# Optimization experiments

Hardware: AMD Instinct MI355X
Metric: run time of the kernel (lower is better)

## Reference

```python
import jax, jax.numpy as jnp
import numpy as np

B, T = 64, 2048
D_RNN, D_EMB, D_ATT = 1024, 512, 128
N_FILT, KSIZE = 32, 31
PAD = (KSIZE - 1) // 2


def setup_inputs() -> dict:
    key = jax.random.key(0)
    ks = jax.random.split(key, 9)
    return {
        "attention_hidden_state": jax.random.normal(ks[0], (B, D_RNN), jnp.float32),
        "memory": jax.random.normal(ks[1], (B, T, D_EMB), jnp.float32),
        "processed_memory": jax.random.normal(ks[2], (B, T, D_ATT), jnp.float32),
        "attention_weights_cat": jax.random.uniform(ks[3], (B, 2, T), jnp.float32),
        "mask": jax.random.randint(ks[4], (B, T), 0, 2) > 0,
        # learned params (all bias-free, as in the torch module)
        "Wq": jax.random.normal(ks[5], (D_ATT, D_RNN), jnp.float32) * 0.02,   # query_layer.weight
        "Wv": jax.random.normal(ks[6], (1, D_ATT), jnp.float32) * 0.02,        # v.weight
        "conv_w": jax.random.normal(ks[7], (N_FILT, 2, KSIZE), jnp.float32) * 0.1,  # location_conv.weight (OIH)
        "Wd": jax.random.normal(ks[8], (D_ATT, N_FILT), jnp.float32) * 0.02,   # location_dense.weight
    }


def reference(attention_hidden_state, memory, processed_memory,
              attention_weights_cat, mask, Wq, Wv, conv_w, Wd):
    # processed query: [B, 1, D_ATT]
    pq = (attention_hidden_state @ Wq.T)[:, None, :]
    # location features: Conv1d(2 -> N_FILT, same padding) over time
    loc = jax.lax.conv_general_dilated(
        attention_weights_cat, conv_w,
        window_strides=(1,), padding=[(PAD, PAD)],
        dimension_numbers=("NCH", "OIH", "NCH"))           # [B, N_FILT, T]
    paw = jnp.einsum("bft,af->bta", loc, Wd)               # [B, T, D_ATT]
    # additive energies -> scalar per position via v-projection
    energies = jnp.einsum("bta,a->bt", jnp.tanh(pq + paw + processed_memory), Wv[0])
    alignment = jnp.where(mask, -jnp.inf, energies)         # masked fill
    attention_weights = jax.nn.softmax(alignment, axis=1)   # [B, T]
    attention_context = jnp.einsum("bt,btd->bd", attention_weights, memory)  # [B, D_EMB]
    return attention_context, jax.lax.stop_gradient(attention_weights)
```

## Files before the change

### kernel.cpp

```cpp
#include <hip/hip_runtime.h>
#include <math.h>

#define B_    64
#define T_    2048
#define DRNN  1024
#define DEMB  512
#define DATT  128
#define NF    32
#define KS    31
#define PADL  15
#define MP    64
#define TT    32
#define CT    64
#define NC    (T_/CT)

__device__ __forceinline__ float fast_tanh(float x){
    float e2 = __expf(2.0f * x);
    return 1.0f - 2.0f / (e2 + 1.0f);
}

__global__ __launch_bounds__(128) void prep_kernel(
    const float* __restrict__ hidden, const float* __restrict__ Wq,
    const float* __restrict__ Wd, const float* __restrict__ convw,
    float* __restrict__ pq, float* __restrict__ M)
{
    const int blk = blockIdx.x;
    const int a = threadIdx.x;
    if (blk < B_) {
        __shared__ float sh[DRNN];
        const int b = blk;
        #pragma unroll
        for (int i = 0; i < DRNN/128; ++i) sh[a + 128*i] = hidden[b*DRNN + a + 128*i];
        __syncthreads();
        const float4* wq4 = (const float4*)(Wq + a*DRNN);
        float acc = 0.f;
        #pragma unroll 4
        for (int k = 0; k < DRNN/4; ++k){
            float4 w = wq4[k];
            acc = fmaf(w.x, sh[4*k+0], acc);
            acc = fmaf(w.y, sh[4*k+1], acc);
            acc = fmaf(w.z, sh[4*k+2], acc);
            acc = fmaf(w.w, sh[4*k+3], acc);
        }
        pq[b*DATT + a] = acc;
    } else {
        float wd[NF];
        #pragma unroll
        for (int f = 0; f < NF; ++f) wd[f] = Wd[a*NF + f];
        for (int ck = 0; ck < 2*KS; ++ck){
            float acc = 0.f;
            #pragma unroll
            for (int f = 0; f < NF; ++f) acc = fmaf(wd[f], convw[f*2*KS + ck], acc);
            M[a*MP + ck] = acc;
        }
    }
}

__global__ __launch_bounds__(256) void fused_kernel(
    const float* __restrict__ pm, const float* __restrict__ awcat,
    const float* __restrict__ pq, const float* __restrict__ M,
    const float* __restrict__ Wv, const int* __restrict__ mask,
    const float* __restrict__ memory,
    float* __restrict__ pbuf, float* __restrict__ pmax,
    float* __restrict__ psum, float* __restrict__ pctx)
{
    const int b   = blockIdx.y;
    const int cx  = blockIdx.x;
    const int t0  = cx * CT;
    const int tid = threadIdx.x;
    const int s   = tid >> 7;
    const int a   = tid & 127;
    const int ts  = t0 + TT * s;

    __shared__ float saw0[96], saw1[96];
    __shared__ float sred[2][2][TT];
    __shared__ float2 swt[CT];
    __shared__ int   scount;
    __shared__ float4 sacc[128];

    for (int i = tid; i < 94; i += 256){
        int tt = t0 - PADL + i;
        bool ok = (tt >= 0) && (tt < T_);
        saw0[i] = ok ? awcat[(b*2+0)*T_ + tt] : 0.f;
        saw1[i] = ok ? awcat[(b*2+1)*T_ + tt] : 0.f;
    }
    __syncthreads();

    const float pqa = pq[b*DATT + a];
    const float wv  = Wv[a];
    const float* pmb = pm + ((size_t)(b*T_ + ts)) * DATT + a;

    float acc[TT];
    #pragma unroll
    for (int t = 0; t < TT; ++t) acc[t] = pqa + pmb[(size_t)t * DATT];

    float Ma0[KS], Ma1[KS];
    const float* Mrow = M + a*MP;
    #pragma unroll
    for (int k = 0; k < KS; ++k){ Ma0[k] = Mrow[k]; Ma1[k] = Mrow[KS + k]; }

    #pragma unroll
    for (int j = 0; j < TT + KS - 1; ++j){
        const float av0 = saw0[j + TT*s];
        const float av1 = saw1[j + TT*s];
        const int tlo = (j - KS + 1) > 0 ? (j - KS + 1) : 0;
        const int thi = (j < TT - 1) ? j : (TT - 1);
        #pragma unroll
        for (int t = tlo; t <= thi; ++t){
            acc[t] = fmaf(Ma0[j - t], av0, acc[t]);
            acc[t] = fmaf(Ma1[j - t], av1, acc[t]);
        }
    }

    #pragma unroll
    for (int t = 0; t < TT; ++t){
        acc[t] = wv * fast_tanh(acc[t]);
    }

    const int lane = tid & 63;
    const int half = a >> 6;
    #pragma unroll
    for (int k = 0; k < 16; ++k){
        const bool hi = (lane & 1) != 0;
        float send = hi ? acc[k] : acc[k+16];
        float recv = __shfl_xor(send, 1, 64);
        acc[k] = (hi ? acc[k+16] : acc[k]) + recv;
    }
    #pragma unroll
    for (int k = 0; k < 8; ++k){
        const bool hi = (lane & 2) != 0;
        float send = hi ? acc[k] : acc[k+8];
        float recv = __shfl_xor(send, 2, 64);
        acc[k] = (hi ? acc[k+8] : acc[k]) + recv;
    }
    #pragma unroll
    for (int k = 0; k < 4; ++k){
        const bool hi = (lane & 4) != 0;
        float send = hi ? acc[k] : acc[k+4];
        float recv = __shfl_xor(send, 4, 64);
        acc[k] = (hi ? acc[k+4] : acc[k]) + recv;
    }
    #pragma unroll
    for (int k = 0; k < 2; ++k){
        const bool hi = (lane & 8) != 0;
        float send = hi ? acc[k] : acc[k+2];
        float recv = __shfl_xor(send, 8, 64);
        acc[k] = (hi ? acc[k+2] : acc[k]) + recv;
    }
    {
        const bool hi = (lane & 16) != 0;
        float send = hi ? acc[0] : acc[1];
        float recv = __shfl_xor(send, 16, 64);
        acc[0] = (hi ? acc[1] : acc[0]) + recv;
    }
    acc[0] += __shfl_xor(acc[0], 32, 64);
    const int trev = ((lane & 1) << 4) | (((lane >> 1) & 1) << 3) |
                     (((lane >> 2) & 1) << 2) | (((lane >> 3) & 1) << 1) |
                     ((lane >> 4) & 1);
    if (lane < 32) sred[s][half][trev] = acc[0];
    __syncthreads();

    if (tid < 64){
        const int t = t0 + tid;
        float e = sred[tid>>5][0][tid&31] + sred[tid>>5][1][tid&31];
        const int mk = mask[b*T_ + t];
        float mval = mk ? -1e30f : e;
        #pragma unroll
        for (int off = 1; off < 64; off <<= 1) mval = fmaxf(mval, __shfl_xor(mval, off, 64));
        const float pval = mk ? 0.f : __expf(e - mval);
        float sv = pval;
        #pragma unroll
        for (int off = 1; off < 64; off <<= 1) sv += __shfl_xor(sv, off, 64);
        pbuf[b*T_ + t] = pval;
        const unsigned long long bal = __ballot(pval != 0.f);
        if (pval != 0.f){
            const int pfx = (int)__popcll(bal & ((1ull << tid) - 1ull));
            swt[pfx] = make_float2(pval, __int_as_float(tid));
        }
        if (tid == 0){
            scount = (int)__popcll(bal);
            pmax[b*NC + cx] = mval;
            psum[b*NC + cx] = sv;
        }
    }
    __syncthreads();

    const int n   = scount;
    const int col = tid & 127;
    const int row = tid >> 7;
    float4 a4 = make_float4(0.f, 0.f, 0.f, 0.f);
    const float4* mem4 = (const float4*)memory + ((size_t)(b*T_ + t0))*(DEMB/4) + col;

    int i = row;
    for (; i + 6 < n; i += 8){
        const float2 e0 = swt[i];
        const float2 e1 = swt[i+2];
        const float2 e2 = swt[i+4];
        const float2 e3 = swt[i+6];
        const float4 m0 = mem4[(size_t)__float_as_int(e0.y) * (DEMB/4)];
        const float4 m1 = mem4[(size_t)__float_as_int(e1.y) * (DEMB/4)];
        const float4 m2 = mem4[(size_t)__float_as_int(e2.y) * (DEMB/4)];
        const float4 m3 = mem4[(size_t)__float_as_int(e3.y) * (DEMB/4)];
        a4.x = fmaf(e0.x, m0.x, a4.x); a4.y = fmaf(e0.x, m0.y, a4.y);
        a4.z = fmaf(e0.x, m0.z, a4.z); a4.w = fmaf(e0.x, m0.w, a4.w);
        a4.x = fmaf(e1.x, m1.x, a4.x); a4.y = fmaf(e1.x, m1.y, a4.y);
        a4.z = fmaf(e1.x, m1.z, a4.z); a4.w = fmaf(e1.x, m1.w, a4.w);
        a4.x = fmaf(e2.x, m2.x, a4.x); a4.y = fmaf(e2.x, m2.y, a4.y);
        a4.z = fmaf(e2.x, m2.z, a4.z); a4.w = fmaf(e2.x, m2.w, a4.w);
        a4.x = fmaf(e3.x, m3.x, a4.x); a4.y = fmaf(e3.x, m3.y, a4.y);
        a4.z = fmaf(e3.x, m3.z, a4.z); a4.w = fmaf(e3.x, m3.w, a4.w);
    }
    for (; i < n; i += 2){
        const float2 e = swt[i];
        const float4 m = mem4[(size_t)__float_as_int(e.y) * (DEMB/4)];
        a4.x = fmaf(e.x, m.x, a4.x); a4.y = fmaf(e.x, m.y, a4.y);
        a4.z = fmaf(e.x, m.z, a4.z); a4.w = fmaf(e.x, m.w, a4.w);
    }

    if (row == 1) sacc[col] = a4;
    __syncthreads();
    if (row == 0){
        const float4 o = sacc[col];
        float4* dst = (float4*)(pctx + ((size_t)(b*NC + cx))*DEMB) + col;
        *dst = make_float4(a4.x + o.x, a4.y + o.y, a4.z + o.z, a4.w + o.w);
    }
}

__global__ __launch_bounds__(256) void finalize_kernel(
    const float* __restrict__ pbuf, const float* __restrict__ pmax,
    const float* __restrict__ psum, const float* __restrict__ pctx,
    float* __restrict__ ctx, float* __restrict__ wout)
{
    const int b = blockIdx.x;
    const int tid = threadIdx.x;
    __shared__ float sscale[NC];

    if (tid < 64){
        float mv = (tid < NC) ? pmax[b*NC + tid] : -1e30f;
        float sv = (tid < NC) ? psum[b*NC + tid] : 0.f;
        float g = mv;
        #pragma unroll
        for (int off = 1; off < 64; off <<= 1) g = fmaxf(g, __shfl_xor(g, off, 64));
        float z = sv * __expf(mv - g);
        #pragma unroll
        for (int off = 1; off < 64; off <<= 1) z += __shfl_xor(z, off, 64);
        if (tid < NC) sscale[tid] = __expf(mv - g) / z;
    }
    __syncthreads();

    float2 a2 = make_float2(0.f, 0.f);
    const float2* pc2 = (const float2*)(pctx + (size_t)b*NC*DEMB) + tid;
    #pragma unroll
    for (int c = 0; c < NC; ++c){
        const float sc = sscale[c];
        if (sc != 0.f){
            const float2 v = pc2[(size_t)c * (DEMB/2)];
            a2.x = fmaf(sc, v.x, a2.x);
            a2.y = fmaf(sc, v.y, a2.y);
        }
    }
    ((float2*)(ctx + b*DEMB))[tid] = a2;

    #pragma unroll
    for (int i = 0; i < T_/256; ++i){
        const int t = tid + 256*i;
        wout[b*T_ + t] = pbuf[b*T_ + t] * sscale[t >> 6];
    }
}

extern "C" void kernel_launch(void* const* d_in, const int* in_sizes, int n_in,
                              void* d_out, int out_size, void* d_ws, size_t ws_size,
                              hipStream_t stream)
{
    const float* hidden = (const float*)d_in[0];
    const float* memory = (const float*)d_in[1];
    const float* pm     = (const float*)d_in[2];
    const float* awcat  = (const float*)d_in[3];
    const int*   mask   = (const int*)d_in[4];
    const float* Wq     = (const float*)d_in[5];
    const float* Wv     = (const float*)d_in[6];
    const float* convw  = (const float*)d_in[7];
    const float* Wd     = (const float*)d_in[8];

    float* out  = (float*)d_out;
    float* ctx  = out;
    float* wout = out + B_*DEMB;

    float* pq    = (float*)d_ws;
    float* M     = pq   + B_*DATT;
    float* pbuf  = M    + DATT*MP;
    float* pmax  = pbuf + B_*T_;
    float* psum  = pmax + B_*NC;
    float* pctx  = psum + B_*NC;

    prep_kernel<<<dim3(B_ + 1), 128, 0, stream>>>(hidden, Wq, Wd, convw, pq, M);
    fused_kernel<<<dim3(NC, B_), 256, 0, stream>>>(pm, awcat, pq, M, Wv, mask,
                                                   memory, pbuf, pmax, psum, pctx);
    finalize_kernel<<<dim3(B_), 256, 0, stream>>>(pbuf, pmax, psum, pctx, ctx, wout);
}
```

Baseline: 441.2 us.

## Skip masked processed_memory loads, transpose conv-dense matrix, warp-parallel query projection

The query projection in the prep kernel now uses one wave per group of 32 outputs, with each lane holding a slice of the hidden state in registers and a shuffle reduction, so Wq rows are read coalesced. The combined conv/dense matrix is stored transposed so each thread's per-attention-dim loads are coalesced across threads. In the fused kernel the mask is read once into a ballot bitmask in shared memory, and the processed_memory loads are skipped for masked positions, which cuts roughly half of that traffic. The memory gather loop is also unrolled to 16 rows so more loads are in flight, at the cost of extra registers.

After: 439.2 us. Within noise of the previous version (-0.5%).

```diff
diff --git a/kernel.cpp b/kernel.cpp
--- a/kernel.cpp
+++ b/kernel.cpp
@@ -9,7 +9,6 @@
 #define NF    32
 #define KS    31
 #define PADL  15
-#define MP    64
 #define TT    32
 #define CT    64
 #define NC    (T_/CT)
@@ -19,46 +18,56 @@
     return 1.0f - 2.0f / (e2 + 1.0f);
 }
 
-__global__ __launch_bounds__(128) void prep_kernel(
+__global__ __launch_bounds__(256) void prep_kernel(
     const float* __restrict__ hidden, const float* __restrict__ Wq,
     const float* __restrict__ Wd, const float* __restrict__ convw,
-    float* __restrict__ pq, float* __restrict__ M)
+    float* __restrict__ pq, float* __restrict__ M2)
 {
     const int blk = blockIdx.x;
-    const int a = threadIdx.x;
+    const int tid = threadIdx.x;
     if (blk < B_) {
-        __shared__ float sh[DRNN];
-        const int b = blk;
-        #pragma unroll
-        for (int i = 0; i < DRNN/128; ++i) sh[a + 128*i] = hidden[b*DRNN + a + 128*i];
-        __syncthreads();
-        const float4* wq4 = (const float4*)(Wq + a*DRNN);
-        float acc = 0.f;
-        #pragma unroll 4
-        for (int k = 0; k < DRNN/4; ++k){
-            float4 w = wq4[k];
-            acc = fmaf(w.x, sh[4*k+0], acc);
-            acc = fmaf(w.y, sh[4*k+1], acc);
-            acc = fmaf(w.z, sh[4*k+2], acc);
-            acc = fmaf(w.w, sh[4*k+3], acc);
-        }
-        pq[b*DATT + a] = acc;
+        const int b    = blk;
+        const int lane = tid & 63;
+        const int w    = tid >> 6;
+        float4 h[4];
+        #pragma unroll
+        for (int j = 0; j < 4; ++j)
+            h[j] = *(const float4*)(hidden + b*DRNN + lane*4 + j*256);
+        for (int ai = 0; ai < 32; ++ai){
+            const int a = w*32 + ai;
+            const float4* wq4 = (const float4*)(Wq + (size_t)a*DRNN);
+            float acc = 0.f;
+            #pragma unroll
+            for (int j = 0; j < 4; ++j){
+                const float4 q = wq4[lane + j*64];
+                acc = fmaf(q.x, h[j].x, acc);
+                acc = fmaf(q.y, h[j].y, acc);
+                acc = fmaf(q.z, h[j].z, acc);
+                acc = fmaf(q.w, h[j].w, acc);
+            }
+            acc += __shfl_xor(acc, 1, 64);  acc += __shfl_xor(acc, 2, 64);
+            acc += __shfl_xor(acc, 4, 64);  acc += __shfl_xor(acc, 8, 64);
+            acc += __shfl_xor(acc, 16, 64); acc += __shfl_xor(acc, 32, 64);
+            if (lane == 0) pq[b*DATT + a] = acc;
+        }
     } else {
+        const int a = tid & 127;
+        const int h = tid >> 7;
         float wd[NF];
         #pragma unroll
         for (int f = 0; f < NF; ++f) wd[f] = Wd[a*NF + f];
-        for (int ck = 0; ck < 2*KS; ++ck){
+        for (int ck = h*KS; ck < h*KS + KS; ++ck){
             float acc = 0.f;
             #pragma unroll
             for (int f = 0; f < NF; ++f) acc = fmaf(wd[f], convw[f*2*KS + ck], acc);
-            M[a*MP + ck] = acc;
+            M2[ck*DATT + a] = acc;
         }
     }
 }
 
 __global__ __launch_bounds__(256) void fused_kernel(
     const float* __restrict__ pm, const float* __restrict__ awcat,
-    const float* __restrict__ pq, const float* __restrict__ M,
+    const float* __restrict__ pq, const float* __restrict__ M2,
     const float* __restrict__ Wv, const int* __restrict__ mask,
     const float* __restrict__ memory,
     float* __restrict__ pbuf, float* __restrict__ pmax,
@@ -77,6 +86,7 @@
     __shared__ float2 swt[CT];
     __shared__ int   scount;
     __shared__ float4 sacc[128];
+    __shared__ unsigned int smkbits[2];
 
     for (int i = tid; i < 94; i += 256){
         int tt = t0 - PADL + i;
@@ -84,20 +94,38 @@
         saw0[i] = ok ? awcat[(b*2+0)*T_ + tt] : 0.f;
         saw1[i] = ok ? awcat[(b*2+1)*T_ + tt] : 0.f;
     }
+    if (tid < 64){
+        const int mk = mask[b*T_ + t0 + tid] != 0;
+        const unsigned long long bal = __ballot(mk);
+        if (tid == 0){
+            smkbits[0] = (unsigned)bal;
+            smkbits[1] = (unsigned)(bal >> 32);
+        }
+    }
     __syncthreads();
 
     const float pqa = pq[b*DATT + a];
     const float wv  = Wv[a];
+    const unsigned mkb = __builtin_amdgcn_readfirstlane(smkbits[s]);
+
     const float* pmb = pm + ((size_t)(b*T_ + ts)) * DATT + a;
-
     float acc[TT];
     #pragma unroll
-    for (int t = 0; t < TT; ++t) acc[t] = pqa + pmb[(size_t)t * DATT];
+    for (int t = 0; t < TT; ++t){
+        acc[t] = 0.f;
+        if (((mkb >> t) & 1u) == 0u) acc[t] = pmb[(size_t)t * DATT];
+    }
 
     float Ma0[KS], Ma1[KS];
-    const float* Mrow = M + a*MP;
-    #pragma unroll
-    for (int k = 0; k < KS; ++k){ Ma0[k] = Mrow[k]; Ma1[k] = Mrow[KS + k]; }
+    const float* M2a = M2 + a;
+    #pragma unroll
+    for (int k = 0; k < KS; ++k){
+        Ma0[k] = M2a[(size_t)k * DATT];
+        Ma1[k] = M2a[(size_t)(KS + k) * DATT];
+    }
+
+    #pragma unroll
+    for (int t = 0; t < TT; ++t) acc[t] += pqa;
 
     #pragma unroll
     for (int j = 0; j < TT + KS - 1; ++j){
@@ -163,7 +191,7 @@
     if (tid < 64){
         const int t = t0 + tid;
         float e = sred[tid>>5][0][tid&31] + sred[tid>>5][1][tid&31];
-        const int mk = mask[b*T_ + t];
+        const int mk = (smkbits[tid>>5] >> (tid&31)) & 1u;
         float mval = mk ? -1e30f : e;
         #pragma unroll
         for (int off = 1; off < 64; off <<= 1) mval = fmaxf(mval, __shfl_xor(mval, off, 64));
@@ -192,6 +220,22 @@
     const float4* mem4 = (const float4*)memory + ((size_t)(b*T_ + t0))*(DEMB/4) + col;
 
     int i = row;
+    for (; i + 14 < n; i += 16){
+        float2 e[8];
+        #pragma unroll
+        for (int u = 0; u < 8; ++u) e[u] = swt[i + 2*u];
+        float4 m[8];
+        #pragma unroll
+        for (int u = 0; u < 8; ++u)
+            m[u] = mem4[(size_t)__float_as_int(e[u].y) * (DEMB/4)];
+        #pragma unroll
+        for (int u = 0; u < 8; ++u){
+            a4.x = fmaf(e[u].x, m[u].x, a4.x);
+            a4.y = fmaf(e[u].x, m[u].y, a4.y);
+            a4.z = fmaf(e[u].x, m[u].z, a4.z);
+            a4.w = fmaf(e[u].x, m[u].w, a4.w);
+        }
+    }
     for (; i + 6 < n; i += 8){
         const float2 e0 = swt[i];
         const float2 e1 = swt[i+2];
@@ -287,14 +331,14 @@
     float* wout = out + B_*DEMB;
 
     float* pq    = (float*)d_ws;
-    float* M     = pq   + B_*DATT;
-    float* pbuf  = M    + DATT*MP;
+    float* M2    = pq   + B_*DATT;
+    float* pbuf  = M2   + 8192;
     float* pmax  = pbuf + B_*T_;
     float* psum  = pmax + B_*NC;
     float* pctx  = psum + B_*NC;
 
-    prep_kernel<<<dim3(B_ + 1), 128, 0, stream>>>(hidden, Wq, Wd, convw, pq, M);
-    fused_kernel<<<dim3(NC, B_), 256, 0, stream>>>(pm, awcat, pq, M, Wv, mask,
+    prep_kernel<<<dim3(B_ + 1), 256, 0, stream>>>(hidden, Wq, Wd, convw, pq, M2);
+    fused_kernel<<<dim3(NC, B_), 256, 0, stream>>>(pm, awcat, pq, M2, Wv, mask,
                                                    memory, pbuf, pmax, psum, pctx);
     finalize_kernel<<<dim3(B_), 256, 0, stream>>>(pbuf, pmax, psum, pctx, ctx, wout);
 }
```
